# Optimization experiments

Hardware: AMD Instinct MI355X
Metric: run time of the kernel (lower is better)

The kernel has to match this reference:

```python
import jax, jax.numpy as jnp
import numpy as np

N_NODES = 40000
N_EDGES = 640000
D_IN = 128
D_HID = 128
D_OUT = 128
N_GRAPHS = 128


def setup_inputs() -> dict:
    key = jax.random.key(0)
    ks = jax.random.split(key, 12)
    x = jax.random.normal(ks[0], (N_NODES, D_IN), dtype=jnp.float32)
    edge_index = jax.random.randint(ks[1], (2, N_EDGES), 0, N_NODES, dtype=jnp.int64)
    batch = jnp.sort(jax.random.randint(ks[2], (N_NODES,), 0, N_GRAPHS, dtype=jnp.int64))
    def lin(k, fan_in, shape):
        s = 1.0 / np.sqrt(fan_in)
        return jax.random.uniform(k, shape, dtype=jnp.float32, minval=-s, maxval=s)
    return {
        "x": x, "edge_index": edge_index, "batch": batch,
        "W_rel0": lin(ks[3], D_IN, (D_IN, D_HID)), "b_rel0": lin(ks[4], D_IN, (D_HID,)), "W_root0": lin(ks[5], D_IN, (D_IN, D_HID)),
        "W_rel1": lin(ks[6], D_HID, (D_HID, D_HID)), "b_rel1": lin(ks[7], D_HID, (D_HID,)), "W_root1": lin(ks[8], D_HID, (D_HID, D_HID)),
        "W_rel2": lin(ks[9], D_HID, (D_HID, D_OUT)), "b_rel2": lin(ks[10], D_HID, (D_OUT,)), "W_root2": lin(ks[11], D_HID, (D_HID, D_OUT)),
    }


def graph_conv(x, src, dst, W_rel, b_rel, W_root):
    # PyG GraphConv: out_i = Lin_rel(sum_{j in N(i)} x_j) + Lin_root(x_i)
    agg = jax.ops.segment_sum(x[src], dst, num_segments=N_NODES)  # [N, F]
    return agg @ W_rel + b_rel + x @ W_root


def reference(x, edge_index, batch,
              W_rel0, b_rel0, W_root0,
              W_rel1, b_rel1, W_root1,
              W_rel2, b_rel2, W_root2):
    src, dst = edge_index[0], edge_index[1]
    h = graph_conv(x, src, dst, W_rel0, b_rel0, W_root0)
    h = jax.nn.relu(h)  # dropout is identity in eval mode
    h = graph_conv(h, src, dst, W_rel1, b_rel1, W_root1)
    h = jax.nn.relu(h)
    h = graph_conv(h, src, dst, W_rel2, b_rel2, W_root2)
    # global_max_pool over per-node graph ids -> [n_graphs, D_OUT]
    return jax.ops.segment_max(h, batch, num_segments=N_GRAPHS)
```

## Files before the change

kernel.cpp:

```cpp
#include <hip/hip_runtime.h>
#include <hip/hip_bf16.h>
#include <math.h>

#define N_NODES 40000
#define N_EDGES 640000
#define D 128
#define N_GRAPHS 128
#define SCAN_NBLK ((N_NODES + 255) / 256)
#define LDS_STRIDE 68

typedef __attribute__((ext_vector_type(8))) short bf16x8;
typedef __attribute__((ext_vector_type(4))) float f32x4;
typedef __attribute__((ext_vector_type(4))) unsigned int u32x4;

static __device__ __forceinline__ unsigned short f2b(float f) {
    unsigned int u = __float_as_uint(f);
    unsigned int r = (u + 0x7fffu + ((u >> 16) & 1u)) >> 16;
    return (unsigned short)r;
}
static __device__ __forceinline__ float b2f(unsigned short h) {
    return __uint_as_float(((unsigned int)h) << 16);
}
static __device__ __forceinline__ float blo(unsigned int u) {
    return __uint_as_float(u << 16);
}
static __device__ __forceinline__ float bhi(unsigned int u) {
    return __uint_as_float(u & 0xffff0000u);
}

__global__ void k_hist(const int* __restrict__ ei, int* __restrict__ counts) {
    int e = blockIdx.x * blockDim.x + threadIdx.x;
    if (e < N_EDGES) atomicAdd(&counts[ei[N_EDGES + e]], 1);
}

__global__ void __launch_bounds__(256) k_scan1(const int* __restrict__ counts,
                                               int* __restrict__ local_pre,
                                               int* __restrict__ blocksums) {
    int t = threadIdx.x;
    int i = blockIdx.x * 256 + t;
    int lane = t & 63, wave = t >> 6;
    int v = (i < N_NODES) ? counts[i] : 0;
    int incl = v;
#pragma unroll
    for (int off = 1; off < 64; off <<= 1) {
        int u = __shfl_up(incl, off);
        if (lane >= off) incl += u;
    }
    __shared__ int ws[4];
    if (lane == 63) ws[wave] = incl;
    __syncthreads();
    int base = 0;
    for (int w = 0; w < 4; ++w) {
        int s = ws[w];
        if (w < wave) base += s;
    }
    if (i < N_NODES) local_pre[i] = base + incl - v;
    if (t == 255) blocksums[blockIdx.x] = base + incl;
}

__global__ void __launch_bounds__(256) k_scan2(int* __restrict__ blocksums) {
    int t = threadIdx.x;
    int lane = t & 63, wave = t >> 6;
    int v = (t < SCAN_NBLK) ? blocksums[t] : 0;
    int incl = v;
#pragma unroll
    for (int off = 1; off < 64; off <<= 1) {
        int u = __shfl_up(incl, off);
        if (lane >= off) incl += u;
    }
    __shared__ int ws[4];
    if (lane == 63) ws[wave] = incl;
    __syncthreads();
    int base = 0;
    for (int w = 0; w < 4; ++w) {
        int s = ws[w];
        if (w < wave) base += s;
    }
    if (t < SCAN_NBLK) blocksums[t] = base + incl - v;
}

__global__ void __launch_bounds__(256) k_scan3(const int* __restrict__ local_pre,
                                               const int* __restrict__ blocksums,
                                               int* __restrict__ row_ptr,
                                               int* __restrict__ cursor) {
    int i = blockIdx.x * 256 + threadIdx.x;
    if (i < N_NODES) {
        int rp = blocksums[blockIdx.x] + local_pre[i];
        row_ptr[i] = rp;
        cursor[i] = rp;
    }
    if (i == 0) row_ptr[N_NODES] = N_EDGES;
}

__global__ void k_scatter(const int* __restrict__ ei, int* __restrict__ cursor,
                          int* __restrict__ src_sorted) {
    int e = blockIdx.x * blockDim.x + threadIdx.x;
    if (e < N_EDGES) {
        int d = ei[N_EDGES + e];
        int pos = atomicAdd(&cursor[d], 1);
        src_sorted[pos] = ei[e];
    }
}

__global__ void k_bounds(const int* __restrict__ batch, int* __restrict__ bounds) {
    int n = blockIdx.x * blockDim.x + threadIdx.x;
    if (n >= N_NODES) return;
    int b = batch[n];
    if (n == 0) {
        for (int g = 0; g <= b; ++g) bounds[g] = 0;
    } else {
        int pb = batch[n - 1];
        for (int g = pb + 1; g <= b; ++g) bounds[g] = n;
    }
    if (n == N_NODES - 1) {
        for (int g = b + 1; g <= N_GRAPHS; ++g) bounds[g] = N_NODES;
    }
}

__global__ void k_x2b(const float* __restrict__ x, unsigned int* __restrict__ xb) {
    int i = blockIdx.x * blockDim.x + threadIdx.x;
    if (i >= N_NODES * D / 8) return;
    const f32x4* xv = (const f32x4*)x;
    f32x4 v0 = xv[i * 2], v1 = xv[i * 2 + 1];
    u32x4 o;
    o.x = ((unsigned int)f2b(v0.y) << 16) | f2b(v0.x);
    o.y = ((unsigned int)f2b(v0.w) << 16) | f2b(v0.z);
    o.z = ((unsigned int)f2b(v1.y) << 16) | f2b(v1.x);
    o.w = ((unsigned int)f2b(v1.w) << 16) | f2b(v1.z);
    ((u32x4*)xb)[i] = o;
}

__global__ void k_wprep3(const float* __restrict__ Wr0, const float* __restrict__ Wt0,
                         const float* __restrict__ Wr1, const float* __restrict__ Wt1,
                         const float* __restrict__ Wr2, const float* __restrict__ Wt2,
                         unsigned short* __restrict__ WT) {
    int l = blockIdx.x >> 7, c = blockIdx.x & 127, k = threadIdx.x;
    const float* Wrel = (l == 0) ? Wr0 : (l == 1) ? Wr1 : Wr2;
    const float* Wroot = (l == 0) ? Wt0 : (l == 1) ? Wt1 : Wt2;
    float v = (k < D) ? Wrel[k * D + c] : Wroot[(k - D) * D + c];
    WT[(size_t)l * 128 * 256 + c * 256 + k] = f2b(v);
}

__global__ void __launch_bounds__(256) k_layer(
    const unsigned short* __restrict__ in,
    const int* __restrict__ row_ptr,
    const int* __restrict__ src_sorted,
    const unsigned short* __restrict__ WT,
    const float* __restrict__ bias,
    unsigned short* __restrict__ out,
    int relu) {
    __shared__ unsigned int aggLDS[16 * LDS_STRIDE];
    int tid = threadIdx.x;
    int w = tid >> 6;
    int lane = tid & 63;
    int g = lane >> 4;
    int c = lane & 15;
    int nodebase = blockIdx.x * 16;
    const u32x4* inv = (const u32x4*)in;

    for (int q = 0; q < 4; ++q) {
        int nl = w * 4 + q;
        int s = row_ptr[nodebase + nl];
        int e = row_ptr[nodebase + nl + 1];

        float a0 = 0.f, a1 = 0.f, a2 = 0.f, a3 = 0.f;
        float a4 = 0.f, a5 = 0.f, a6 = 0.f, a7 = 0.f;
        int j = s;
        for (; j + 8 <= e; j += 8) {
            int sn0 = src_sorted[j + g];
            int sn1 = src_sorted[j + 4 + g];
            u32x4 v0 = inv[sn0 * 16 + c];
            u32x4 v1 = inv[sn1 * 16 + c];
            a0 += blo(v0.x); a1 += bhi(v0.x);
            a2 += blo(v0.y); a3 += bhi(v0.y);
            a4 += blo(v0.z); a5 += bhi(v0.z);
            a6 += blo(v0.w); a7 += bhi(v0.w);
            a0 += blo(v1.x); a1 += bhi(v1.x);
            a2 += blo(v1.y); a3 += bhi(v1.y);
            a4 += blo(v1.z); a5 += bhi(v1.z);
            a6 += blo(v1.w); a7 += bhi(v1.w);
        }
        for (; j < e; j += 4) {
            int jj = j + g;
            if (jj < e) {
                int sn = src_sorted[jj];
                u32x4 v = inv[sn * 16 + c];
                a0 += blo(v.x); a1 += bhi(v.x);
                a2 += blo(v.y); a3 += bhi(v.y);
                a4 += blo(v.z); a5 += bhi(v.z);
                a6 += blo(v.w); a7 += bhi(v.w);
            }
        }
        a0 += __shfl_xor(a0, 16); a0 += __shfl_xor(a0, 32);
        a1 += __shfl_xor(a1, 16); a1 += __shfl_xor(a1, 32);
        a2 += __shfl_xor(a2, 16); a2 += __shfl_xor(a2, 32);
        a3 += __shfl_xor(a3, 16); a3 += __shfl_xor(a3, 32);
        a4 += __shfl_xor(a4, 16); a4 += __shfl_xor(a4, 32);
        a5 += __shfl_xor(a5, 16); a5 += __shfl_xor(a5, 32);
        a6 += __shfl_xor(a6, 16); a6 += __shfl_xor(a6, 32);
        a7 += __shfl_xor(a7, 16); a7 += __shfl_xor(a7, 32);

        float lo_f, hi_f;
        if (g == 0)      { lo_f = a0; hi_f = a1; }
        else if (g == 1) { lo_f = a2; hi_f = a3; }
        else if (g == 2) { lo_f = a4; hi_f = a5; }
        else             { lo_f = a6; hi_f = a7; }
        unsigned int o = ((unsigned int)f2b(hi_f) << 16) | (unsigned int)f2b(lo_f);
        aggLDS[nl * LDS_STRIDE + c * 4 + g] = o;
    }
    __syncthreads();

    int row = c, quad = g;
    int colbase = w * 32;

    f32x4 acc0 = {0.f, 0.f, 0.f, 0.f};
    f32x4 acc1 = {0.f, 0.f, 0.f, 0.f};

    const unsigned int* Al = &aggLDS[row * LDS_STRIDE];
    const short* Xp = (const short*)(in + (nodebase + row) * D);
    const short* W0 = (const short*)(WT + (colbase + row) * 256);
    const short* W1 = (const short*)(WT + (colbase + 16 + row) * 256);

#pragma unroll
    for (int s = 0; s < 4; ++s) {
        bf16x8 af = *(const bf16x8*)(Al + s * 16 + quad * 4);
        int k0 = s * 32 + quad * 8;
        bf16x8 b0 = *(const bf16x8*)(W0 + k0);
        bf16x8 b1 = *(const bf16x8*)(W1 + k0);
        acc0 = __builtin_amdgcn_mfma_f32_16x16x32_bf16(af, b0, acc0, 0, 0, 0);
        acc1 = __builtin_amdgcn_mfma_f32_16x16x32_bf16(af, b1, acc1, 0, 0, 0);
    }
#pragma unroll
    for (int s = 0; s < 4; ++s) {
        int k0 = s * 32 + quad * 8;
        bf16x8 xf = *(const bf16x8*)(Xp + k0);
        bf16x8 b0 = *(const bf16x8*)(W0 + 128 + k0);
        bf16x8 b1 = *(const bf16x8*)(W1 + 128 + k0);
        acc0 = __builtin_amdgcn_mfma_f32_16x16x32_bf16(xf, b0, acc0, 0, 0, 0);
        acc1 = __builtin_amdgcn_mfma_f32_16x16x32_bf16(xf, b1, acc1, 0, 0, 0);
    }

    int c0 = colbase + row, c1 = c0 + 16;
    float bia0 = bias[c0], bia1 = bias[c1];
#pragma unroll
    for (int r = 0; r < 4; ++r) {
        int n2 = nodebase + quad * 4 + r;
        float v0 = acc0[r] + bia0;
        float v1 = acc1[r] + bia1;
        if (relu) { v0 = fmaxf(v0, 0.f); v1 = fmaxf(v1, 0.f); }
        out[n2 * D + c0] = f2b(v0);
        out[n2 * D + c1] = f2b(v1);
    }
}

__global__ void __launch_bounds__(512) k_segmax(const unsigned short* __restrict__ h,
                                                const int* __restrict__ bounds,
                                                float* __restrict__ out) {
    __shared__ float sm[8][128];
    int g = blockIdx.x;
    int tid = threadIdx.x;
    int rg = tid >> 6;
    int c = tid & 63;
    int s = bounds[g], e = bounds[g + 1];
    const unsigned int* h32 = (const unsigned int*)h;

    float m0 = -INFINITY, m1 = -INFINITY;
    int n = s + rg;
    for (; n + 8 < e; n += 16) {
        unsigned int v0 = h32[n * 64 + c];
        unsigned int v1 = h32[(n + 8) * 64 + c];
        m0 = fmaxf(m0, blo(v0)); m1 = fmaxf(m1, bhi(v0));
        m0 = fmaxf(m0, blo(v1)); m1 = fmaxf(m1, bhi(v1));
    }
    if (n < e) {
        unsigned int v0 = h32[n * 64 + c];
        m0 = fmaxf(m0, blo(v0)); m1 = fmaxf(m1, bhi(v0));
    }
    sm[rg][c * 2] = m0;
    sm[rg][c * 2 + 1] = m1;
    __syncthreads();
    if (tid < 128) {
        float m = sm[0][tid];
#pragma unroll
        for (int r = 1; r < 8; ++r) m = fmaxf(m, sm[r][tid]);
        out[g * D + tid] = m;
    }
}

extern "C" void kernel_launch(void* const* d_in, const int* in_sizes, int n_in,
                              void* d_out, int out_size, void* d_ws, size_t ws_size,
                              hipStream_t stream) {
    const float* x = (const float*)d_in[0];
    const int* ei = (const int*)d_in[1];
    const int* batch = (const int*)d_in[2];
    const float* Wrel[3]  = {(const float*)d_in[3], (const float*)d_in[6], (const float*)d_in[9]};
    const float* brel[3]  = {(const float*)d_in[4], (const float*)d_in[7], (const float*)d_in[10]};
    const float* Wroot[3] = {(const float*)d_in[5], (const float*)d_in[8], (const float*)d_in[11]};
    float* out = (float*)d_out;

    char* ws = (char*)d_ws;
    size_t off = 0;
    auto alloc = [&](size_t bytes) -> void* {
        void* p = ws + off;
        off = (off + bytes + 255) & ~(size_t)255;
        return p;
    };
    unsigned short* xb  = (unsigned short*)alloc((size_t)N_NODES * D * 2);
    unsigned short* hA  = (unsigned short*)alloc((size_t)N_NODES * D * 2);
    unsigned short* hB  = (unsigned short*)alloc((size_t)N_NODES * D * 2);
    unsigned short* WT  = (unsigned short*)alloc((size_t)3 * 128 * 256 * 2);
    int* row_ptr    = (int*)alloc((size_t)(N_NODES + 1) * 4);
    int* cursor     = (int*)alloc((size_t)N_NODES * 4);
    int* src_sorted = (int*)alloc((size_t)N_EDGES * 4);
    int* bounds     = (int*)alloc((size_t)(N_GRAPHS + 1) * 4);
    int* local_pre  = (int*)alloc((size_t)N_NODES * 4);
    int* blocksums  = (int*)alloc((size_t)SCAN_NBLK * 4);

    hipMemsetAsync(cursor, 0, (size_t)N_NODES * 4, stream);
    k_hist<<<(N_EDGES + 255) / 256, 256, 0, stream>>>(ei, cursor);
    k_scan1<<<SCAN_NBLK, 256, 0, stream>>>(cursor, local_pre, blocksums);
    k_scan2<<<1, 256, 0, stream>>>(blocksums);
    k_scan3<<<SCAN_NBLK, 256, 0, stream>>>(local_pre, blocksums, row_ptr, cursor);
    k_scatter<<<(N_EDGES + 255) / 256, 256, 0, stream>>>(ei, cursor, src_sorted);
    k_bounds<<<(N_NODES + 255) / 256, 256, 0, stream>>>(batch, bounds);

    k_x2b<<<(N_NODES * D / 8 + 255) / 256, 256, 0, stream>>>(x, (unsigned int*)xb);
    k_wprep3<<<384, 256, 0, stream>>>(Wrel[0], Wroot[0], Wrel[1], Wroot[1],
                                      Wrel[2], Wroot[2], WT);

    const unsigned short* in = xb;
    unsigned short* houts[3] = {hA, hB, hA};
    for (int l = 0; l < 3; ++l) {
        k_layer<<<N_NODES / 16, 256, 0, stream>>>(in, row_ptr, src_sorted,
                                                  WT + (size_t)l * 128 * 256,
                                                  brel[l], houts[l], (l < 2) ? 1 : 0);
        in = houts[l];
    }

    k_segmax<<<N_GRAPHS, 512, 0, stream>>>(houts[2], bounds, out);
}
```

Baseline: 313.8 us.

## Pad CSR neighbor lists to multiples of eight and gather with one node per quarter-wave

Pads each node's neighbor list to a multiple of 8 using a zero dummy row (index N_NODES), adding a k_pad kernel and an extra zeroed row in each feature buffer. The aggregation kernel now assigns one node per 16-lane group instead of looping over four nodes per wave. Each lane loads eight indices with two int4 loads and issues eight independent row gathers per trip, so no tail loop or cross-group shuffle reduction is needed. This removes the branchy remainder handling and reduction shuffles and raises memory-level parallelism. The cost is extra gather traffic for padding entries, plus load imbalance between the groups in a wave because node degrees differ.

```diff
diff --git a/kernel.cpp b/kernel.cpp
--- a/kernel.cpp
+++ b/kernel.cpp
@@ -18,9 +18,6 @@
     unsigned int r = (u + 0x7fffu + ((u >> 16) & 1u)) >> 16;
     return (unsigned short)r;
 }
-static __device__ __forceinline__ float b2f(unsigned short h) {
-    return __uint_as_float(((unsigned int)h) << 16);
-}
 static __device__ __forceinline__ float blo(unsigned int u) {
     return __uint_as_float(u << 16);
 }
@@ -39,7 +36,7 @@
     int t = threadIdx.x;
     int i = blockIdx.x * 256 + t;
     int lane = t & 63, wave = t >> 6;
-    int v = (i < N_NODES) ? counts[i] : 0;
+    int v = (i < N_NODES) ? ((counts[i] + 7) & ~7) : 0;
     int incl = v;
 #pragma unroll
     for (int off = 1; off < 64; off <<= 1) {
@@ -81,25 +78,34 @@
 
 __global__ void __launch_bounds__(256) k_scan3(const int* __restrict__ local_pre,
                                                const int* __restrict__ blocksums,
-                                               int* __restrict__ row_ptr,
+                                               const int* __restrict__ counts,
+                                               int* __restrict__ rp_pad,
                                                int* __restrict__ cursor) {
     int i = blockIdx.x * 256 + threadIdx.x;
     if (i < N_NODES) {
         int rp = blocksums[blockIdx.x] + local_pre[i];
-        row_ptr[i] = rp;
+        rp_pad[i] = rp;
         cursor[i] = rp;
-    }
-    if (i == 0) row_ptr[N_NODES] = N_EDGES;
+        if (i == N_NODES - 1) rp_pad[N_NODES] = rp + ((counts[i] + 7) & ~7);
+    }
 }
 
 __global__ void k_scatter(const int* __restrict__ ei, int* __restrict__ cursor,
-                          int* __restrict__ src_sorted) {
+                          int* __restrict__ src_pad) {
     int e = blockIdx.x * blockDim.x + threadIdx.x;
     if (e < N_EDGES) {
         int d = ei[N_EDGES + e];
         int pos = atomicAdd(&cursor[d], 1);
-        src_sorted[pos] = ei[e];
-    }
+        src_pad[pos] = ei[e];
+    }
+}
+
+__global__ void k_pad(const int* __restrict__ cursor, const int* __restrict__ rp_pad,
+                      int* __restrict__ src_pad) {
+    int i = blockIdx.x * blockDim.x + threadIdx.x;
+    if (i >= N_NODES) return;
+    int s = cursor[i], e = rp_pad[i + 1];
+    for (int j = s; j < e; ++j) src_pad[j] = N_NODES;
 }
 
 __global__ void k_bounds(const int* __restrict__ batch, int* __restrict__ bounds) {
@@ -143,8 +149,8 @@
 
 __global__ void __launch_bounds__(256) k_layer(
     const unsigned short* __restrict__ in,
-    const int* __restrict__ row_ptr,
-    const int* __restrict__ src_sorted,
+    const int* __restrict__ rp_pad,
+    const int* __restrict__ src_pad,
     const unsigned short* __restrict__ WT,
     const float* __restrict__ bias,
     unsigned short* __restrict__ out,
@@ -153,64 +159,51 @@
     int tid = threadIdx.x;
     int w = tid >> 6;
     int lane = tid & 63;
-    int g = lane >> 4;
+    int q = lane >> 4;
     int c = lane & 15;
+    int nl = w * 4 + q;
     int nodebase = blockIdx.x * 16;
     const u32x4* inv = (const u32x4*)in;
 
-    for (int q = 0; q < 4; ++q) {
-        int nl = w * 4 + q;
-        int s = row_ptr[nodebase + nl];
-        int e = row_ptr[nodebase + nl + 1];
-
-        float a0 = 0.f, a1 = 0.f, a2 = 0.f, a3 = 0.f;
-        float a4 = 0.f, a5 = 0.f, a6 = 0.f, a7 = 0.f;
-        int j = s;
-        for (; j + 8 <= e; j += 8) {
-            int sn0 = src_sorted[j + g];
-            int sn1 = src_sorted[j + 4 + g];
-            u32x4 v0 = inv[sn0 * 16 + c];
-            u32x4 v1 = inv[sn1 * 16 + c];
-            a0 += blo(v0.x); a1 += bhi(v0.x);
-            a2 += blo(v0.y); a3 += bhi(v0.y);
-            a4 += blo(v0.z); a5 += bhi(v0.z);
-            a6 += blo(v0.w); a7 += bhi(v0.w);
-            a0 += blo(v1.x); a1 += bhi(v1.x);
-            a2 += blo(v1.y); a3 += bhi(v1.y);
-            a4 += blo(v1.z); a5 += bhi(v1.z);
-            a6 += blo(v1.w); a7 += bhi(v1.w);
-        }
-        for (; j < e; j += 4) {
-            int jj = j + g;
-            if (jj < e) {
-                int sn = src_sorted[jj];
-                u32x4 v = inv[sn * 16 + c];
-                a0 += blo(v.x); a1 += bhi(v.x);
-                a2 += blo(v.y); a3 += bhi(v.y);
-                a4 += blo(v.z); a5 += bhi(v.z);
-                a6 += blo(v.w); a7 += bhi(v.w);
-            }
-        }
-        a0 += __shfl_xor(a0, 16); a0 += __shfl_xor(a0, 32);
-        a1 += __shfl_xor(a1, 16); a1 += __shfl_xor(a1, 32);
-        a2 += __shfl_xor(a2, 16); a2 += __shfl_xor(a2, 32);
-        a3 += __shfl_xor(a3, 16); a3 += __shfl_xor(a3, 32);
-        a4 += __shfl_xor(a4, 16); a4 += __shfl_xor(a4, 32);
-        a5 += __shfl_xor(a5, 16); a5 += __shfl_xor(a5, 32);
-        a6 += __shfl_xor(a6, 16); a6 += __shfl_xor(a6, 32);
-        a7 += __shfl_xor(a7, 16); a7 += __shfl_xor(a7, 32);
-
-        float lo_f, hi_f;
-        if (g == 0)      { lo_f = a0; hi_f = a1; }
-        else if (g == 1) { lo_f = a2; hi_f = a3; }
-        else if (g == 2) { lo_f = a4; hi_f = a5; }
-        else             { lo_f = a6; hi_f = a7; }
-        unsigned int o = ((unsigned int)f2b(hi_f) << 16) | (unsigned int)f2b(lo_f);
-        aggLDS[nl * LDS_STRIDE + c * 4 + g] = o;
-    }
+    int s = rp_pad[nodebase + nl];
+    int e = rp_pad[nodebase + nl + 1];
+    const int4* sidx = (const int4*)(src_pad + s);
+    int ntrips = (e - s) >> 3;
+
+    float a0 = 0.f, a1 = 0.f, a2 = 0.f, a3 = 0.f;
+    float a4 = 0.f, a5 = 0.f, a6 = 0.f, a7 = 0.f;
+
+#define ACC8(v) do { \
+        a0 += blo((v).x); a1 += bhi((v).x); \
+        a2 += blo((v).y); a3 += bhi((v).y); \
+        a4 += blo((v).z); a5 += bhi((v).z); \
+        a6 += blo((v).w); a7 += bhi((v).w); } while (0)
+
+    for (int t = 0; t < ntrips; ++t) {
+        int4 ia = sidx[2 * t];
+        int4 ib = sidx[2 * t + 1];
+        u32x4 v0 = inv[ia.x * 16 + c];
+        u32x4 v1 = inv[ia.y * 16 + c];
+        u32x4 v2 = inv[ia.z * 16 + c];
+        u32x4 v3 = inv[ia.w * 16 + c];
+        u32x4 v4 = inv[ib.x * 16 + c];
+        u32x4 v5 = inv[ib.y * 16 + c];
+        u32x4 v6 = inv[ib.z * 16 + c];
+        u32x4 v7 = inv[ib.w * 16 + c];
+        ACC8(v0); ACC8(v1); ACC8(v2); ACC8(v3);
+        ACC8(v4); ACC8(v5); ACC8(v6); ACC8(v7);
+    }
+#undef ACC8
+
+    u32x4 o;
+    o.x = ((unsigned int)f2b(a1) << 16) | f2b(a0);
+    o.y = ((unsigned int)f2b(a3) << 16) | f2b(a2);
+    o.z = ((unsigned int)f2b(a5) << 16) | f2b(a4);
+    o.w = ((unsigned int)f2b(a7) << 16) | f2b(a6);
+    *(u32x4*)&aggLDS[nl * LDS_STRIDE + c * 4] = o;
     __syncthreads();
 
-    int row = c, quad = g;
+    int row = c, quad = q;
     int colbase = w * 32;
 
     f32x4 acc0 = {0.f, 0.f, 0.f, 0.f};
@@ -222,17 +215,17 @@
     const short* W1 = (const short*)(WT + (colbase + 16 + row) * 256);
 
 #pragma unroll
-    for (int s = 0; s < 4; ++s) {
-        bf16x8 af = *(const bf16x8*)(Al + s * 16 + quad * 4);
-        int k0 = s * 32 + quad * 8;
+    for (int t = 0; t < 4; ++t) {
+        bf16x8 af = *(const bf16x8*)(Al + t * 16 + quad * 4);
+        int k0 = t * 32 + quad * 8;
         bf16x8 b0 = *(const bf16x8*)(W0 + k0);
         bf16x8 b1 = *(const bf16x8*)(W1 + k0);
         acc0 = __builtin_amdgcn_mfma_f32_16x16x32_bf16(af, b0, acc0, 0, 0, 0);
         acc1 = __builtin_amdgcn_mfma_f32_16x16x32_bf16(af, b1, acc1, 0, 0, 0);
     }
 #pragma unroll
-    for (int s = 0; s < 4; ++s) {
-        int k0 = s * 32 + quad * 8;
+    for (int t = 0; t < 4; ++t) {
+        int k0 = t * 32 + quad * 8;
         bf16x8 xf = *(const bf16x8*)(Xp + k0);
         bf16x8 b0 = *(const bf16x8*)(W0 + 128 + k0);
         bf16x8 b1 = *(const bf16x8*)(W1 + 128 + k0);
@@ -305,23 +298,29 @@
         off = (off + bytes + 255) & ~(size_t)255;
         return p;
     };
-    unsigned short* xb  = (unsigned short*)alloc((size_t)N_NODES * D * 2);
-    unsigned short* hA  = (unsigned short*)alloc((size_t)N_NODES * D * 2);
-    unsigned short* hB  = (unsigned short*)alloc((size_t)N_NODES * D * 2);
+    unsigned short* xb  = (unsigned short*)alloc((size_t)(N_NODES + 1) * D * 2);
+    unsigned short* hA  = (unsigned short*)alloc((size_t)(N_NODES + 1) * D * 2);
+    unsigned short* hB  = (unsigned short*)alloc((size_t)(N_NODES + 1) * D * 2);
     unsigned short* WT  = (unsigned short*)alloc((size_t)3 * 128 * 256 * 2);
-    int* row_ptr    = (int*)alloc((size_t)(N_NODES + 1) * 4);
+    int* rp_pad     = (int*)alloc((size_t)(N_NODES + 1) * 4);
+    int* counts     = (int*)alloc((size_t)N_NODES * 4);
     int* cursor     = (int*)alloc((size_t)N_NODES * 4);
-    int* src_sorted = (int*)alloc((size_t)N_EDGES * 4);
+    int* src_pad    = (int*)alloc((size_t)(N_EDGES + 8 * N_NODES) * 4);
     int* bounds     = (int*)alloc((size_t)(N_GRAPHS + 1) * 4);
     int* local_pre  = (int*)alloc((size_t)N_NODES * 4);
     int* blocksums  = (int*)alloc((size_t)SCAN_NBLK * 4);
 
-    hipMemsetAsync(cursor, 0, (size_t)N_NODES * 4, stream);
-    k_hist<<<(N_EDGES + 255) / 256, 256, 0, stream>>>(ei, cursor);
-    k_scan1<<<SCAN_NBLK, 256, 0, stream>>>(cursor, local_pre, blocksums);
+    hipMemsetAsync(counts, 0, (size_t)N_NODES * 4, stream);
+    hipMemsetAsync(xb + (size_t)N_NODES * D, 0, D * 2, stream);
+    hipMemsetAsync(hA + (size_t)N_NODES * D, 0, D * 2, stream);
+    hipMemsetAsync(hB + (size_t)N_NODES * D, 0, D * 2, stream);
+
+    k_hist<<<(N_EDGES + 255) / 256, 256, 0, stream>>>(ei, counts);
+    k_scan1<<<SCAN_NBLK, 256, 0, stream>>>(counts, local_pre, blocksums);
     k_scan2<<<1, 256, 0, stream>>>(blocksums);
-    k_scan3<<<SCAN_NBLK, 256, 0, stream>>>(local_pre, blocksums, row_ptr, cursor);
-    k_scatter<<<(N_EDGES + 255) / 256, 256, 0, stream>>>(ei, cursor, src_sorted);
+    k_scan3<<<SCAN_NBLK, 256, 0, stream>>>(local_pre, blocksums, counts, rp_pad, cursor);
+    k_scatter<<<(N_EDGES + 255) / 256, 256, 0, stream>>>(ei, cursor, src_pad);
+    k_pad<<<SCAN_NBLK, 256, 0, stream>>>(cursor, rp_pad, src_pad);
     k_bounds<<<(N_NODES + 255) / 256, 256, 0, stream>>>(batch, bounds);
 
     k_x2b<<<(N_NODES * D / 8 + 255) / 256, 256, 0, stream>>>(x, (unsigned int*)xb);
@@ -331,7 +330,7 @@
     const unsigned short* in = xb;
     unsigned short* houts[3] = {hA, hB, hA};
     for (int l = 0; l < 3; ++l) {
-        k_layer<<<N_NODES / 16, 256, 0, stream>>>(in, row_ptr, src_sorted,
+        k_layer<<<N_NODES / 16, 256, 0, stream>>>(in, rp_pad, src_pad,
                                                   WT + (size_t)l * 128 * 256,
                                                   brel[l], houts[l], (l < 2) ? 1 : 0);
         in = houts[l];
```

Measured after the change: 295.6 us. 5.8% less time.
